# Kernel tuning notes

Measured on AMD Instinct MI355X. Metric: run time of the kernel, lower is better.

Reference implementation:

```python
import jax, jax.numpy as jnp
import numpy as np

N, XDIM, D, K = 400000, 128, 3, 4
TWO_PI = 2.0 * np.pi


def _scaled(k, shape):
    fan_in = shape[0]
    return jax.random.normal(k, shape, jnp.float32) * np.float32(1.0 / np.sqrt(fan_in))


def setup_inputs() -> dict:
    key = jax.random.key(0)
    ks = jax.random.split(key, 9)
    return {
        "x1": jax.random.normal(ks[0], (N, XDIM), jnp.float32),
        "enc_w1": _scaled(ks[1], (XDIM, 16)), "enc_b1": jnp.zeros((16,), jnp.float32),
        "enc_w2": _scaled(ks[2], (16, 8)),   "enc_b2": jnp.zeros((8,), jnp.float32),
        "enc_w3": _scaled(ks[3], (8, 1)),    "enc_b3": jnp.zeros((1,), jnp.float32),
        "dec_w1": _scaled(ks[4], (1, 8)),    "dec_b1": jnp.zeros((8,), jnp.float32),
        "dec_w2": _scaled(ks[5], (8, 16)),   "dec_b2": jnp.zeros((16,), jnp.float32),
        "dec_w3": _scaled(ks[6], (16, XDIM)),"dec_b3": jnp.zeros((XDIM,), jnp.float32),
        "est_w1": _scaled(ks[7], (D, 8)),    "est_b1": jnp.zeros((8,), jnp.float32),
        "est_w2": _scaled(ks[8], (8, K)),    "est_b2": jnp.zeros((K,), jnp.float32),
    }


def reference(x1, enc_w1, enc_b1, enc_w2, enc_b2, enc_w3, enc_b3,
              dec_w1, dec_b1, dec_w2, dec_b2, dec_w3, dec_b3,
              est_w1, est_b1, est_w2, est_b2):
    # encoder: Dense(16,tanh)->Dense(8,tanh)->Dense(1,tanh)
    h = jnp.tanh(x1 @ enc_w1 + enc_b1)
    h = jnp.tanh(h @ enc_w2 + enc_b2)
    z1 = jnp.tanh(h @ enc_w3 + enc_b3)            # [N,1]
    # decoder: Dense(8,tanh)->Dense(16,tanh)->Dense(xdim, linear)
    h = jnp.tanh(z1 @ dec_w1 + dec_b1)
    h = jnp.tanh(h @ dec_w2 + dec_b2)
    x2 = h @ dec_w3 + dec_b3                      # [N,xdim]

    # relative distances
    dist_cos = jnp.sum(x1 * x2, axis=1, keepdims=True) / (
        jnp.linalg.norm(x1, axis=1, keepdims=True) * jnp.linalg.norm(x2, axis=1, keepdims=True))
    dist_euc = jnp.linalg.norm(x1 - x2, axis=1, keepdims=True)
    z = jnp.concatenate([z1, dist_cos, dist_euc], axis=1)   # [N,D]

    # estimator: Dense(8,tanh)->Dense(K,softmax)
    gamma = jax.nn.softmax(jnp.tanh(z @ est_w1 + est_b1) @ est_w2 + est_b2)  # [N,K]

    # GMM parameters from soft assignments
    gamma_sum = jnp.sum(gamma, axis=0)                        # [K]
    phi = jnp.mean(gamma, axis=0)                             # [K]
    mu = jnp.einsum('ik,il->kl', gamma, z) / gamma_sum[:, None]          # [K,D]
    z_centered = jnp.sqrt(gamma)[:, :, None] * (z[:, None, :] - mu[None, :, :])  # [N,K,D]
    sigma = jnp.einsum('ikl,ikm->klm', z_centered, z_centered) / gamma_sum[:, None, None]  # [K,D,D]

    # per-sample energy
    z_mu = z[:, None, :] - mu[None, :, :]                     # [N,K,D]
    sigma_inv = jnp.linalg.inv(sigma)                         # [K,D,D]
    item1 = jnp.log(phi)[None, :]                             # [1,K]
    item2 = -0.5 * jnp.einsum('nkd,kde,nke->nk', z_mu, sigma_inv, z_mu)  # [N,K]
    sigma_det = jnp.linalg.det(TWO_PI * sigma)                # [K]
    item3 = jnp.log(jnp.sqrt(sigma_det))[None, :]             # [1,K]
    energy = -jnp.sum(item1 + item2 - item3, axis=1)          # [N]

    # loss
    lambda1, lambda2 = 0.01, 0.0001
    diag = jnp.diagonal(sigma, axis1=-2, axis2=-1)            # [K,D]
    loss3 = lambda2 * jnp.sum(1.0 / diag)
    loss2 = lambda1 * jnp.mean(energy)
    loss1 = jnp.mean(jnp.sum(jnp.square(x1 - x2), axis=1))
    loss = loss1 + loss2 + loss3
    return energy, loss
```

## Files before the change

### kernel.cpp

```cpp
#include <hip/hip_runtime.h>

#define NSAMP 400000
#define NBLK  1563


__device__ __forceinline__ float ftanh(float x) {
    float e = __expf(2.0f * x);
    return 1.0f - __fdividef(2.0f, e + 1.0f);
}

__global__ __launch_bounds__(256) void prep_kernel(const float* __restrict__ dw3,
                                                   const float* __restrict__ db3,
                                                   float* __restrict__ Gm,
                                                   float* __restrict__ gv,
                                                   float* __restrict__ bb) {
    __shared__ float sw3[2048];
    __shared__ float sb3[128];
    int t = threadIdx.x;
    for (int k = t; k < 2048; k += 256) sw3[k] = dw3[k];
    if (t < 128) sb3[t] = db3[t];
    __syncthreads();
    int a = t >> 4, b = t & 15;
    float s = 0.f;
    for (int j = 0; j < 128; ++j) s = fmaf(sw3[a * 128 + j], sw3[b * 128 + j], s);
    Gm[t] = s;
    if (t < 16) {
        float sg = 0.f;
        for (int j = 0; j < 128; ++j) sg = fmaf(sw3[t * 128 + j], sb3[j], sg);
        gv[t] = sg;
    }
    if (t == 0) {
        float sbv = 0.f;
        for (int j = 0; j < 128; ++j) sbv = fmaf(sb3[j], sb3[j], sbv);
        *bb = sbv;
    }
}

__global__ __launch_bounds__(256) void pass1_kernel(
    const float* __restrict__ x1,
    const float* __restrict__ ew1, const float* __restrict__ eb1,
    const float* __restrict__ ew2, const float* __restrict__ eb2,
    const float* __restrict__ ew3, const float* __restrict__ eb3,
    const float* __restrict__ dw1, const float* __restrict__ db1,
    const float* __restrict__ dw2, const float* __restrict__ db2,
    const float* __restrict__ dw3, const float* __restrict__ db3,
    const float* __restrict__ tw1, const float* __restrict__ tb1,
    const float* __restrict__ tw2, const float* __restrict__ tb2,
    const float* __restrict__ Gm, const float* __restrict__ gv,
    const float* __restrict__ bbp,
    double* __restrict__ acc, float4* __restrict__ zbuf) {
    __shared__ float4 lbuf[2048];
    __shared__ float sPart[4][41];

    int t = threadIdx.x;
    int i = blockIdx.x * 256 + t;
    bool active = (i < NSAMP);
    int bbase = blockIdx.x * 256;
    int w = t >> 6, lane = t & 63;
    int sw2 = (t >> 1) & 3;
    const float4* x1f4 = (const float4*)x1;

    const float4* p[4];
#pragma unroll
    for (int c2 = 0; c2 < 4; ++c2) {
        int idx = (w * 4 + c2) * 64 + lane;
        int row = idx >> 2, qs = idx & 3;
        int q = qs ^ ((row >> 1) & 3);
        int grow = bbase + row;
        if (grow >= NSAMP) grow = NSAMP - 1;
        p[c2] = x1f4 + (size_t)grow * 32 + q;
    }

#pragma unroll
    for (int c2 = 0; c2 < 4; ++c2) {
        __builtin_amdgcn_global_load_lds(
            (const __attribute__((address_space(1))) void*)p[c2],
            (__attribute__((address_space(3))) void*)(lbuf + (w * 4 + c2) * 64),
            16, 0, 0);
        p[c2] += 4;
    }

    float u[16], v[16];
#pragma unroll
    for (int k = 0; k < 16; ++k) { u[k] = 0.f; v[k] = 0.f; }
    float s2 = 0.f, sb = 0.f;

    auto consume = [&](int blk, int bofs) {
        float xe[16];
#pragma unroll
        for (int q = 0; q < 4; ++q) {
            float4 w4 = lbuf[bofs + t * 4 + (q ^ sw2)];
            xe[q * 4 + 0] = w4.x; xe[q * 4 + 1] = w4.y;
            xe[q * 4 + 2] = w4.z; xe[q * 4 + 3] = w4.w;
        }
        int j0 = blk * 16;
#pragma unroll
        for (int e = 0; e < 16; ++e) {
            float x = xe[e];
            s2 = fmaf(x, x, s2);
            sb = fmaf(x, db3[j0 + e], sb);
#pragma unroll
            for (int k = 0; k < 16; ++k) u[k] = fmaf(x, ew1[(j0 + e) * 16 + k], u[k]);
        }
#pragma unroll
        for (int q = 0; q < 16; ++q) {
            float a2 = v[q];
#pragma unroll
            for (int e = 0; e < 16; ++e) a2 = fmaf(xe[e], dw3[q * 128 + j0 + e], a2);
            v[q] = a2;
        }
    };

#pragma unroll 1
    for (int blk = 0; blk < 7; ++blk) {
        int nb = ((blk + 1) & 1) * 1024;
#pragma unroll
        for (int c2 = 0; c2 < 4; ++c2) {
            __builtin_amdgcn_global_load_lds(
                (const __attribute__((address_space(1))) void*)p[c2],
                (__attribute__((address_space(3))) void*)(lbuf + nb + (w * 4 + c2) * 64),
                16, 0, 0);
            p[c2] += 4;
        }
        asm volatile("s_waitcnt vmcnt(4)" ::: "memory");
        __builtin_amdgcn_sched_barrier(0);
        consume(blk, (blk & 1) * 1024);
    }
    asm volatile("s_waitcnt vmcnt(0)" ::: "memory");
    __builtin_amdgcn_sched_barrier(0);
    consume(7, 1024);

    float h1[16];
#pragma unroll
    for (int k = 0; k < 16; ++k) h1[k] = ftanh(u[k] + eb1[k]);
    float h2[8];
#pragma unroll
    for (int m = 0; m < 8; ++m) {
        float a2 = eb2[m];
#pragma unroll
        for (int k = 0; k < 16; ++k) a2 = fmaf(h1[k], ew2[k * 8 + m], a2);
        h2[m] = ftanh(a2);
    }
    float a3 = eb3[0];
#pragma unroll
    for (int m = 0; m < 8; ++m) a3 = fmaf(h2[m], ew3[m], a3);
    float z1 = ftanh(a3);

    float d1[8];
#pragma unroll
    for (int p2 = 0; p2 < 8; ++p2) d1[p2] = ftanh(fmaf(z1, dw1[p2], db1[p2]));
    float d2[16];
#pragma unroll
    for (int q = 0; q < 16; ++q) {
        float a2 = db2[q];
#pragma unroll
        for (int p2 = 0; p2 < 8; ++p2) a2 = fmaf(d1[p2], dw2[p2 * 16 + q], a2);
        d2[q] = ftanh(a2);
    }

    float dot = sb;
#pragma unroll
    for (int q = 0; q < 16; ++q) dot = fmaf(d2[q], v[q], dot);
    float n2 = *bbp;
#pragma unroll
    for (int a = 0; a < 16; ++a) {
        float ra = 2.0f * gv[a];
#pragma unroll
        for (int b = 0; b < 16; ++b) ra = fmaf(Gm[a * 16 + b], d2[b], ra);
        n2 = fmaf(d2[a], ra, n2);
    }
    n2 = fmaxf(n2, 1e-20f);
    float euc2 = fmaxf(s2 - 2.0f * dot + n2, 0.f);
    float deuc = sqrtf(euc2);
    float dcos = dot * rsqrtf(s2 * n2);

    float zf[3] = {z1, dcos, deuc};

    float e1[8];
#pragma unroll
    for (int p2 = 0; p2 < 8; ++p2) {
        float a2 = tb1[p2];
        a2 = fmaf(zf[0], tw1[0 * 8 + p2], a2);
        a2 = fmaf(zf[1], tw1[1 * 8 + p2], a2);
        a2 = fmaf(zf[2], tw1[2 * 8 + p2], a2);
        e1[p2] = ftanh(a2);
    }
    float lg[4];
#pragma unroll
    for (int k = 0; k < 4; ++k) {
        float a2 = tb2[k];
#pragma unroll
        for (int p2 = 0; p2 < 8; ++p2) a2 = fmaf(e1[p2], tw2[p2 * 4 + k], a2);
        lg[k] = a2;
    }
    float mx = fmaxf(fmaxf(lg[0], lg[1]), fmaxf(lg[2], lg[3]));
    float ex[4]; float se = 0.f;
#pragma unroll
    for (int k = 0; k < 4; ++k) { ex[k] = __expf(lg[k] - mx); se += ex[k]; }
    float inv = __fdividef(1.0f, se);
    float gam[4];
#pragma unroll
    for (int k = 0; k < 4; ++k) gam[k] = ex[k] * inv;

    if (active) zbuf[i] = make_float4(zf[0], zf[1], zf[2], 0.f);
    if (!active) { gam[0] = gam[1] = gam[2] = gam[3] = 0.f; euc2 = 0.f; }

    int rlane = threadIdx.x & 63;
    int wid = threadIdx.x >> 6;

#define REDUCE_STORE(T, VAL) { float _v = (VAL);                          \
        _v += __shfl_down(_v, 32); _v += __shfl_down(_v, 16);             \
        _v += __shfl_down(_v, 8);  _v += __shfl_down(_v, 4);              \
        _v += __shfl_down(_v, 2);  _v += __shfl_down(_v, 1);              \
        if (rlane == 0) sPart[wid][T] = _v; }

#pragma unroll
    for (int k = 0; k < 4; ++k) REDUCE_STORE(k, gam[k]);
#pragma unroll
    for (int k = 0; k < 4; ++k) {
#pragma unroll
        for (int d = 0; d < 3; ++d) REDUCE_STORE(4 + k * 3 + d, gam[k] * zf[d]);
    }
#pragma unroll
    for (int k = 0; k < 4; ++k) {
        REDUCE_STORE(16 + k * 6 + 0, gam[k] * zf[0] * zf[0]);
        REDUCE_STORE(16 + k * 6 + 1, gam[k] * zf[0] * zf[1]);
        REDUCE_STORE(16 + k * 6 + 2, gam[k] * zf[0] * zf[2]);
        REDUCE_STORE(16 + k * 6 + 3, gam[k] * zf[1] * zf[1]);
        REDUCE_STORE(16 + k * 6 + 4, gam[k] * zf[1] * zf[2]);
        REDUCE_STORE(16 + k * 6 + 5, gam[k] * zf[2] * zf[2]);
    }
    REDUCE_STORE(40, euc2);
#undef REDUCE_STORE

    __syncthreads();
    if (threadIdx.x < 41) {
        double s = (double)sPart[0][threadIdx.x] + (double)sPart[1][threadIdx.x]
                 + (double)sPart[2][threadIdx.x] + (double)sPart[3][threadIdx.x];
        unsafeAtomicAdd(&acc[threadIdx.x], s);
    }
}

__global__ void gmm_kernel(double* __restrict__ acc, float* __restrict__ P) {
    if (threadIdx.x != 0 || blockIdx.x != 0) return;
    double M[6] = {0, 0, 0, 0, 0, 0}, bv[3] = {0, 0, 0}, A = 0.0, loss3 = 0.0;
    const double TWO_PI = 6.283185307179586;
    for (int k = 0; k < 4; ++k) {
        double g = acc[k];
        double phi = g / (double)NSAMP;
        double mu0 = acc[4 + k * 3 + 0] / g;
        double mu1 = acc[4 + k * 3 + 1] / g;
        double mu2 = acc[4 + k * 3 + 2] / g;
        double S00 = acc[16 + k * 6 + 0] / g - mu0 * mu0;
        double S01 = acc[16 + k * 6 + 1] / g - mu0 * mu1;
        double S02 = acc[16 + k * 6 + 2] / g - mu0 * mu2;
        double S11 = acc[16 + k * 6 + 3] / g - mu1 * mu1;
        double S12 = acc[16 + k * 6 + 4] / g - mu1 * mu2;
        double S22 = acc[16 + k * 6 + 5] / g - mu2 * mu2;
        double c00 = S11 * S22 - S12 * S12;
        double c01 = S02 * S12 - S01 * S22;
        double c02 = S01 * S12 - S02 * S11;
        double det = S00 * c00 + S01 * c01 + S02 * c02;
        double id = 1.0 / det;
        double I00 = c00 * id, I01 = c01 * id, I02 = c02 * id;
        double I11 = (S00 * S22 - S02 * S02) * id;
        double I12 = (S01 * S02 - S00 * S12) * id;
        double I22 = (S00 * S11 - S01 * S01) * id;
        M[0] += I00; M[1] += I01; M[2] += I02; M[3] += I11; M[4] += I12; M[5] += I22;
        double b0 = I00 * mu0 + I01 * mu1 + I02 * mu2;
        double b1 = I01 * mu0 + I11 * mu1 + I12 * mu2;
        double b2 = I02 * mu0 + I12 * mu1 + I22 * mu2;
        bv[0] += b0; bv[1] += b1; bv[2] += b2;
        double quad = mu0 * b0 + mu1 * b1 + mu2 * b2;
        A += -log(phi) + 0.5 * log(TWO_PI * TWO_PI * TWO_PI * det) + 0.5 * quad;
        loss3 += 1e-4 * (1.0 / S00 + 1.0 / S11 + 1.0 / S22);
    }
    P[0] = (float)M[0]; P[1] = (float)M[1]; P[2] = (float)M[2];
    P[3] = (float)M[3]; P[4] = (float)M[4]; P[5] = (float)M[5];
    P[6] = (float)bv[0]; P[7] = (float)bv[1]; P[8] = (float)bv[2];
    P[9] = (float)A;
    acc[42] = acc[40] / (double)NSAMP + loss3;
}

__global__ __launch_bounds__(256) void energy_kernel(const float4* __restrict__ zbuf,
                                                     const float* __restrict__ P,
                                                     double* __restrict__ acc,
                                                     unsigned* __restrict__ cnt,
                                                     float* __restrict__ out) {
    int i = blockIdx.x * 256 + threadIdx.x;
    float e = 0.f;
    if (i < NSAMP) {
        float4 z4 = zbuf[i];
        float z0 = z4.x, z1 = z4.y, z2 = z4.z;
        float q = P[0] * z0 * z0 + P[3] * z1 * z1 + P[5] * z2 * z2
                + 2.f * (P[1] * z0 * z1 + P[2] * z0 * z2 + P[4] * z1 * z2);
        e = P[9] + 0.5f * q - (P[6] * z0 + P[7] * z1 + P[8] * z2);
        out[i] = e;
    }
    float s = e;
    s += __shfl_down(s, 32); s += __shfl_down(s, 16); s += __shfl_down(s, 8);
    s += __shfl_down(s, 4);  s += __shfl_down(s, 2);  s += __shfl_down(s, 1);
    __shared__ float sE[4];
    if ((threadIdx.x & 63) == 0) sE[threadIdx.x >> 6] = s;
    __syncthreads();
    if (threadIdx.x == 0) {
        double t = (double)sE[0] + (double)sE[1] + (double)sE[2] + (double)sE[3];
        unsafeAtomicAdd(&acc[41], t);
        __threadfence();
        unsigned old = atomicAdd(cnt, 1u);
        if (old == (unsigned)(NBLK - 1)) {
            double tot = unsafeAtomicAdd(&acc[41], 0.0);
            out[NSAMP] = (float)(acc[42] + 0.01 * tot / (double)NSAMP);
        }
    }
}

extern "C" void kernel_launch(void* const* d_in, const int* in_sizes, int n_in,
                              void* d_out, int out_size, void* d_ws, size_t ws_size,
                              hipStream_t stream) {
    const float* x1  = (const float*)d_in[0];
    const float* ew1 = (const float*)d_in[1];
    const float* eb1 = (const float*)d_in[2];
    const float* ew2 = (const float*)d_in[3];
    const float* eb2 = (const float*)d_in[4];
    const float* ew3 = (const float*)d_in[5];
    const float* eb3 = (const float*)d_in[6];
    const float* dw1 = (const float*)d_in[7];
    const float* db1 = (const float*)d_in[8];
    const float* dw2 = (const float*)d_in[9];
    const float* db2 = (const float*)d_in[10];
    const float* dw3 = (const float*)d_in[11];
    const float* db3 = (const float*)d_in[12];
    const float* tw1 = (const float*)d_in[13];
    const float* tb1 = (const float*)d_in[14];
    const float* tw2 = (const float*)d_in[15];
    const float* tb2 = (const float*)d_in[16];
    float* out = (float*)d_out;
    char* ws = (char*)d_ws;
    double* acc   = (double*)ws;
    unsigned* cnt = (unsigned*)(ws + 352);
    float* P    = (float*)(ws + 384);
    float* Gm   = (float*)(ws + 1024);
    float* gv   = (float*)(ws + 2048);
    float* bb   = (float*)(ws + 2112);
    float4* zb  = (float4*)(ws + 4096);

    hipMemsetAsync(d_ws, 0, 512, stream);
    prep_kernel<<<1, 256, 0, stream>>>(dw3, db3, Gm, gv, bb);
    pass1_kernel<<<NBLK, 256, 0, stream>>>(x1, ew1, eb1, ew2, eb2, ew3, eb3,
                                           dw1, db1, dw2, db2, dw3, db3,
                                           tw1, tb1, tw2, tb2, Gm, gv, bb, acc, zb);
    gmm_kernel<<<1, 64, 0, stream>>>(acc, P);
    energy_kernel<<<NBLK, 256, 0, stream>>>(zb, P, acc, cnt, out);
}
```

Before: 471.3 us.

## Stage MLP weights in LDS with float4 reads and spread atomic accumulators

New measurement: 456.7 us. 1.03x faster.

```diff
diff --git a/kernel.cpp b/kernel.cpp
--- a/kernel.cpp
+++ b/kernel.cpp
@@ -51,6 +51,18 @@
     double* __restrict__ acc, float4* __restrict__ zbuf) {
     __shared__ float4 lbuf[2048];
     __shared__ float sPart[4][41];
+    __shared__ __align__(16) float sEw1[2048];
+    __shared__ __align__(16) float sDw3[2048];
+    __shared__ __align__(16) float sGm[256];
+    __shared__ __align__(16) float sDb3[128];
+    __shared__ __align__(16) float sEw2[128];
+    __shared__ __align__(16) float sDw2[128];
+    __shared__ __align__(16) float sTw1[24];
+    __shared__ __align__(16) float sTw2[32];
+    __shared__ float sGv[16], sEb1[16], sDb2[16];
+    __shared__ float sEb2[8], sEw3[8], sDw1[8], sDb1[8], sTb1[8];
+    __shared__ float sTb2[4];
+    __shared__ float sBb, sEb3;
 
     int t = threadIdx.x;
     int i = blockIdx.x * 256 + t;
@@ -70,7 +82,6 @@
         if (grow >= NSAMP) grow = NSAMP - 1;
         p[c2] = x1f4 + (size_t)grow * 32 + q;
     }
-
 #pragma unroll
     for (int c2 = 0; c2 < 4; ++c2) {
         __builtin_amdgcn_global_load_lds(
@@ -80,6 +91,27 @@
         p[c2] += 4;
     }
 
+    for (int k = t; k < 2048; k += 256) { sEw1[k] = ew1[k]; sDw3[k] = dw3[k]; }
+    sGm[t & 255] = Gm[t & 255];
+    if (t < 128) { sDb3[t] = db3[t]; sEw2[t] = ew2[t]; sDw2[t] = dw2[t]; }
+    if (t < 16) { sGv[t] = gv[t]; sEb1[t] = eb1[t]; sDb2[t] = db2[t]; }
+    if (t < 8) { sEb2[t] = eb2[t]; sEw3[t] = ew3[t]; sDw1[t] = dw1[t];
+                 sDb1[t] = db1[t]; sTb1[t] = tb1[t]; }
+    if (t < 24) sTw1[t] = tw1[t];
+    if (t < 32) sTw2[t] = tw2[t];
+    if (t < 4) sTb2[t] = tb2[t];
+    if (t == 0) { sBb = *bbp; sEb3 = eb3[0]; }
+    __syncthreads();
+
+    const float4* sEw1_4 = (const float4*)sEw1;
+    const float4* sDw3_4 = (const float4*)sDw3;
+    const float4* sDb3_4 = (const float4*)sDb3;
+    const float4* sGm_4  = (const float4*)sGm;
+    const float4* sEw2_4 = (const float4*)sEw2;
+    const float4* sDw2_4 = (const float4*)sDw2;
+    const float4* sTw1_4 = (const float4*)sTw1;
+    const float4* sTw2_4 = (const float4*)sTw2;
+
     float u[16], v[16];
 #pragma unroll
     for (int k = 0; k < 16; ++k) { u[k] = 0.f; v[k] = 0.f; }
@@ -95,18 +127,36 @@
         }
         int j0 = blk * 16;
 #pragma unroll
+        for (int ee = 0; ee < 4; ++ee) {
+            float4 bv = sDb3_4[(j0 >> 2) + ee];
+            s2 = fmaf(xe[ee*4+0], xe[ee*4+0], s2); sb = fmaf(xe[ee*4+0], bv.x, sb);
+            s2 = fmaf(xe[ee*4+1], xe[ee*4+1], s2); sb = fmaf(xe[ee*4+1], bv.y, sb);
+            s2 = fmaf(xe[ee*4+2], xe[ee*4+2], s2); sb = fmaf(xe[ee*4+2], bv.z, sb);
+            s2 = fmaf(xe[ee*4+3], xe[ee*4+3], s2); sb = fmaf(xe[ee*4+3], bv.w, sb);
+        }
+#pragma unroll
         for (int e = 0; e < 16; ++e) {
             float x = xe[e];
-            s2 = fmaf(x, x, s2);
-            sb = fmaf(x, db3[j0 + e], sb);
-#pragma unroll
-            for (int k = 0; k < 16; ++k) u[k] = fmaf(x, ew1[(j0 + e) * 16 + k], u[k]);
+#pragma unroll
+            for (int kk = 0; kk < 4; ++kk) {
+                float4 wv = sEw1_4[(j0 + e) * 4 + kk];
+                u[kk*4+0] = fmaf(x, wv.x, u[kk*4+0]);
+                u[kk*4+1] = fmaf(x, wv.y, u[kk*4+1]);
+                u[kk*4+2] = fmaf(x, wv.z, u[kk*4+2]);
+                u[kk*4+3] = fmaf(x, wv.w, u[kk*4+3]);
+            }
         }
 #pragma unroll
         for (int q = 0; q < 16; ++q) {
             float a2 = v[q];
 #pragma unroll
-            for (int e = 0; e < 16; ++e) a2 = fmaf(xe[e], dw3[q * 128 + j0 + e], a2);
+            for (int ee = 0; ee < 4; ++ee) {
+                float4 wv = sDw3_4[q * 32 + (j0 >> 2) + ee];
+                a2 = fmaf(xe[ee*4+0], wv.x, a2);
+                a2 = fmaf(xe[ee*4+1], wv.y, a2);
+                a2 = fmaf(xe[ee*4+2], wv.z, a2);
+                a2 = fmaf(xe[ee*4+3], wv.w, a2);
+            }
             v[q] = a2;
         }
     };
@@ -132,41 +182,62 @@
 
     float h1[16];
 #pragma unroll
-    for (int k = 0; k < 16; ++k) h1[k] = ftanh(u[k] + eb1[k]);
+    for (int k = 0; k < 16; ++k) h1[k] = ftanh(u[k] + sEb1[k]);
+    float a2m[8];
+#pragma unroll
+    for (int m = 0; m < 8; ++m) a2m[m] = sEb2[m];
+#pragma unroll
+    for (int k = 0; k < 16; ++k) {
+        float4 r0 = sEw2_4[k * 2], r1 = sEw2_4[k * 2 + 1];
+        a2m[0] = fmaf(h1[k], r0.x, a2m[0]); a2m[1] = fmaf(h1[k], r0.y, a2m[1]);
+        a2m[2] = fmaf(h1[k], r0.z, a2m[2]); a2m[3] = fmaf(h1[k], r0.w, a2m[3]);
+        a2m[4] = fmaf(h1[k], r1.x, a2m[4]); a2m[5] = fmaf(h1[k], r1.y, a2m[5]);
+        a2m[6] = fmaf(h1[k], r1.z, a2m[6]); a2m[7] = fmaf(h1[k], r1.w, a2m[7]);
+    }
     float h2[8];
 #pragma unroll
-    for (int m = 0; m < 8; ++m) {
-        float a2 = eb2[m];
-#pragma unroll
-        for (int k = 0; k < 16; ++k) a2 = fmaf(h1[k], ew2[k * 8 + m], a2);
-        h2[m] = ftanh(a2);
-    }
-    float a3 = eb3[0];
-#pragma unroll
-    for (int m = 0; m < 8; ++m) a3 = fmaf(h2[m], ew3[m], a3);
+    for (int m = 0; m < 8; ++m) h2[m] = ftanh(a2m[m]);
+    float a3 = sEb3;
+#pragma unroll
+    for (int m = 0; m < 8; ++m) a3 = fmaf(h2[m], sEw3[m], a3);
     float z1 = ftanh(a3);
 
     float d1[8];
 #pragma unroll
-    for (int p2 = 0; p2 < 8; ++p2) d1[p2] = ftanh(fmaf(z1, dw1[p2], db1[p2]));
+    for (int p2 = 0; p2 < 8; ++p2) d1[p2] = ftanh(fmaf(z1, sDw1[p2], sDb1[p2]));
+    float a2q[16];
+#pragma unroll
+    for (int q = 0; q < 16; ++q) a2q[q] = sDb2[q];
+#pragma unroll
+    for (int p2 = 0; p2 < 8; ++p2) {
+#pragma unroll
+        for (int q4 = 0; q4 < 4; ++q4) {
+            float4 r = sDw2_4[p2 * 4 + q4];
+            a2q[q4*4+0] = fmaf(d1[p2], r.x, a2q[q4*4+0]);
+            a2q[q4*4+1] = fmaf(d1[p2], r.y, a2q[q4*4+1]);
+            a2q[q4*4+2] = fmaf(d1[p2], r.z, a2q[q4*4+2]);
+            a2q[q4*4+3] = fmaf(d1[p2], r.w, a2q[q4*4+3]);
+        }
+    }
     float d2[16];
 #pragma unroll
-    for (int q = 0; q < 16; ++q) {
-        float a2 = db2[q];
-#pragma unroll
-        for (int p2 = 0; p2 < 8; ++p2) a2 = fmaf(d1[p2], dw2[p2 * 16 + q], a2);
-        d2[q] = ftanh(a2);
-    }
+    for (int q = 0; q < 16; ++q) d2[q] = ftanh(a2q[q]);
 
     float dot = sb;
 #pragma unroll
     for (int q = 0; q < 16; ++q) dot = fmaf(d2[q], v[q], dot);
-    float n2 = *bbp;
+    float n2 = sBb;
 #pragma unroll
     for (int a = 0; a < 16; ++a) {
-        float ra = 2.0f * gv[a];
-#pragma unroll
-        for (int b = 0; b < 16; ++b) ra = fmaf(Gm[a * 16 + b], d2[b], ra);
+        float ra = 2.0f * sGv[a];
+#pragma unroll
+        for (int b4 = 0; b4 < 4; ++b4) {
+            float4 g = sGm_4[a * 4 + b4];
+            ra = fmaf(g.x, d2[b4*4+0], ra);
+            ra = fmaf(g.y, d2[b4*4+1], ra);
+            ra = fmaf(g.z, d2[b4*4+2], ra);
+            ra = fmaf(g.w, d2[b4*4+3], ra);
+        }
         n2 = fmaf(d2[a], ra, n2);
     }
     n2 = fmaxf(n2, 1e-20f);
@@ -176,22 +247,28 @@
 
     float zf[3] = {z1, dcos, deuc};
 
+    float e1a[8];
+#pragma unroll
+    for (int p2 = 0; p2 < 8; ++p2) e1a[p2] = sTb1[p2];
+#pragma unroll
+    for (int d = 0; d < 3; ++d) {
+        float4 r0 = sTw1_4[d * 2], r1 = sTw1_4[d * 2 + 1];
+        e1a[0] = fmaf(zf[d], r0.x, e1a[0]); e1a[1] = fmaf(zf[d], r0.y, e1a[1]);
+        e1a[2] = fmaf(zf[d], r0.z, e1a[2]); e1a[3] = fmaf(zf[d], r0.w, e1a[3]);
+        e1a[4] = fmaf(zf[d], r1.x, e1a[4]); e1a[5] = fmaf(zf[d], r1.y, e1a[5]);
+        e1a[6] = fmaf(zf[d], r1.z, e1a[6]); e1a[7] = fmaf(zf[d], r1.w, e1a[7]);
+    }
     float e1[8];
 #pragma unroll
+    for (int p2 = 0; p2 < 8; ++p2) e1[p2] = ftanh(e1a[p2]);
+    float lg[4];
+#pragma unroll
+    for (int k = 0; k < 4; ++k) lg[k] = sTb2[k];
+#pragma unroll
     for (int p2 = 0; p2 < 8; ++p2) {
-        float a2 = tb1[p2];
-        a2 = fmaf(zf[0], tw1[0 * 8 + p2], a2);
-        a2 = fmaf(zf[1], tw1[1 * 8 + p2], a2);
-        a2 = fmaf(zf[2], tw1[2 * 8 + p2], a2);
-        e1[p2] = ftanh(a2);
-    }
-    float lg[4];
-#pragma unroll
-    for (int k = 0; k < 4; ++k) {
-        float a2 = tb2[k];
-#pragma unroll
-        for (int p2 = 0; p2 < 8; ++p2) a2 = fmaf(e1[p2], tw2[p2 * 4 + k], a2);
-        lg[k] = a2;
+        float4 r = sTw2_4[p2];
+        lg[0] = fmaf(e1[p2], r.x, lg[0]); lg[1] = fmaf(e1[p2], r.y, lg[1]);
+        lg[2] = fmaf(e1[p2], r.z, lg[2]); lg[3] = fmaf(e1[p2], r.w, lg[3]);
     }
     float mx = fmaxf(fmaxf(lg[0], lg[1]), fmaxf(lg[2], lg[3]));
     float ex[4]; float se = 0.f;
@@ -237,12 +314,18 @@
     if (threadIdx.x < 41) {
         double s = (double)sPart[0][threadIdx.x] + (double)sPart[1][threadIdx.x]
                  + (double)sPart[2][threadIdx.x] + (double)sPart[3][threadIdx.x];
-        unsafeAtomicAdd(&acc[threadIdx.x], s);
+        double* accs = acc + (size_t)(blockIdx.x & 7) * 48;
+        unsafeAtomicAdd(&accs[threadIdx.x], s);
     }
 }
 
 __global__ void gmm_kernel(double* __restrict__ acc, float* __restrict__ P) {
     if (threadIdx.x != 0 || blockIdx.x != 0) return;
+    for (int j = 0; j < 42; ++j) {
+        double s = acc[j];
+        for (int c = 1; c < 8; ++c) s += acc[c * 48 + j];
+        acc[j] = s;
+    }
     double M[6] = {0, 0, 0, 0, 0, 0}, bv[3] = {0, 0, 0}, A = 0.0, loss3 = 0.0;
     const double TWO_PI = 6.283185307179586;
     for (int k = 0; k < 4; ++k) {
@@ -305,11 +388,14 @@
     __syncthreads();
     if (threadIdx.x == 0) {
         double t = (double)sE[0] + (double)sE[1] + (double)sE[2] + (double)sE[3];
-        unsafeAtomicAdd(&acc[41], t);
+        double* accs = acc + (size_t)(blockIdx.x & 7) * 48;
+        unsafeAtomicAdd(&accs[41], t);
         __threadfence();
         unsigned old = atomicAdd(cnt, 1u);
         if (old == (unsigned)(NBLK - 1)) {
-            double tot = unsafeAtomicAdd(&acc[41], 0.0);
+            double tot = 0.0;
+            for (int c = 0; c < 8; ++c)
+                tot += unsafeAtomicAdd(&acc[c * 48 + 41], 0.0);
             out[NSAMP] = (float)(acc[42] + 0.01 * tot / (double)NSAMP);
         }
     }
@@ -338,14 +424,14 @@
     float* out = (float*)d_out;
     char* ws = (char*)d_ws;
     double* acc   = (double*)ws;
-    unsigned* cnt = (unsigned*)(ws + 352);
-    float* P    = (float*)(ws + 384);
-    float* Gm   = (float*)(ws + 1024);
-    float* gv   = (float*)(ws + 2048);
-    float* bb   = (float*)(ws + 2112);
-    float4* zb  = (float4*)(ws + 4096);
-
-    hipMemsetAsync(d_ws, 0, 512, stream);
+    unsigned* cnt = (unsigned*)(ws + 3072);
+    float* P    = (float*)(ws + 3584);
+    float* Gm   = (float*)(ws + 4096);
+    float* gv   = (float*)(ws + 5120);
+    float* bb   = (float*)(ws + 5184);
+    float4* zb  = (float4*)(ws + 8192);
+
+    hipMemsetAsync(d_ws, 0, 3584, stream);
     prep_kernel<<<1, 256, 0, stream>>>(dw3, db3, Gm, gv, bb);
     pass1_kernel<<<NBLK, 256, 0, stream>>>(x1, ew1, eb1, ew2, eb2, ew3, eb3,
                                            dw1, db1, dw2, db2, dw3, db3,
```
